# Kernel tuning notes

Measured on AMD Instinct MI355X. Metric: run time of the kernel, lower is better.

The kernel has to match this reference:

```python
import jax, jax.numpy as jnp
import numpy as np

N_NODES = 100000
DEGREE = 16
FEAT = 128
HID = 64
OUT = 16
BATCH = 4096
K = 12  # n_neibs


def setup_inputs() -> dict:
    key = jax.random.key(0)
    ks = jax.random.split(key, 12)
    idx0 = jax.random.randint(ks[0], (BATCH,), 0, N_NODES, dtype=jnp.int64 if jax.config.jax_enable_x64 else jnp.int32)
    buf1 = jax.random.randint(ks[1], (BATCH, K), 0, 1000000)
    buf2 = jax.random.randint(ks[2], (BATCH * K, K), 0, 1000000)
    indptr = jnp.arange(N_NODES) * DEGREE            # CSR row pointers (fixed degree)
    indices = jax.random.randint(ks[3], (N_NODES * DEGREE,), 0, N_NODES)
    degrees = jnp.full((N_NODES,), DEGREE, dtype=jnp.int32)
    emb_weight = jax.random.normal(ks[4], (N_NODES, FEAT), dtype=jnp.float32)
    enc_w = jax.random.normal(ks[5], (HID, FEAT), dtype=jnp.float32) * (1.0 / np.sqrt(FEAT))
    h1_w = jax.random.normal(ks[6], (HID, 2 * HID), dtype=jnp.float32) * (1.0 / np.sqrt(2 * HID))
    h1_b = jnp.zeros((HID,), jnp.float32)
    h2_w = jax.random.normal(ks[7], (HID, HID), dtype=jnp.float32) * (1.0 / np.sqrt(HID))
    h2_b = jnp.zeros((HID,), jnp.float32)
    out_w = jax.random.normal(ks[8], (OUT, HID), dtype=jnp.float32) * (1.0 / np.sqrt(HID))
    out_b = jnp.zeros((OUT,), jnp.float32)
    return dict(idx0=idx0, buf1=buf1, buf2=buf2, indptr=indptr, indices=indices,
                degrees=degrees, emb_weight=emb_weight, enc_w=enc_w,
                h1_w=h1_w, h1_b=h1_b, h2_w=h2_w, h2_b=h2_b, out_w=out_w, out_b=out_b)


def _sample_neighbors(nodes, buf, indptr, indices, degrees):
    # nodes: [M], buf: [M, K] random ints -> neighbor node ids [M, K]
    neibs = buf % degrees[nodes][:, None]
    offsets = indptr[nodes][:, None] + neibs
    return indices[offsets]


def reference(idx0, buf1, buf2, indptr, indices, degrees, emb_weight,
              enc_w, h1_w, h1_b, h2_w, h2_b, out_w, out_b):
    B = idx0.shape[0]
    idx1 = _sample_neighbors(idx0, buf1, indptr, indices, degrees)              # [B, K]
    idx2 = _sample_neighbors(idx1.reshape(B * K), buf2, indptr, indices, degrees)
    idx2 = idx2.reshape(B, K, K)                                                # [B, K, K]

    enc_1hop = jax.nn.relu(jnp.einsum('bkf,hf->bkh', emb_weight[idx1], enc_w))  # [B, K, H]
    enc_2hop = jax.nn.relu(jnp.einsum('bkjf,hf->bkjh', emb_weight[idx2], enc_w))
    avg_2hop = enc_2hop.mean(axis=-2)                                           # [B, K, H]

    h1 = jnp.concatenate([enc_1hop, avg_2hop], axis=-1)                         # [B, K, 2H]
    h1 = jax.nn.relu(jnp.einsum('bkc,hc->bkh', h1, h1_w) + h1_b)
    avg_1hop = h1.mean(axis=-2)                                                 # [B, H]
    h0 = jax.nn.relu(avg_1hop @ h2_w.T + h2_b)
    return h0 @ out_w.T + out_b                                                 # [B, OUT]
```

## Files before the change

kernel.cpp:

```cpp
#include <hip/hip_runtime.h>

#define NNODES 100000

typedef __attribute__((ext_vector_type(8))) short bf16x8;
typedef __attribute__((ext_vector_type(4))) float floatx4;

union PackU { uint4 u; bf16x8 v; };

__device__ __forceinline__ uint pack_hi2(float x0, float x1) {
    return (__float_as_uint(x1) & 0xFFFF0000u) | (__float_as_uint(x0) >> 16);
}
__device__ __forceinline__ uint pack_lo2(float x0, float x1) {
    float l0 = x0 - __uint_as_float(__float_as_uint(x0) & 0xFFFF0000u);
    float l1 = x1 - __uint_as_float(__float_as_uint(x1) & 0xFFFF0000u);
    return (__float_as_uint(l1) & 0xFFFF0000u) | (__float_as_uint(l0) >> 16);
}
__device__ __forceinline__ ushort bf_rne(float x) {
    unsigned u = __float_as_uint(x);
    return (ushort)((u + 0x7FFFu + ((u >> 16) & 1u)) >> 16);
}
__device__ __forceinline__ float lo16f(uint u) { return __uint_as_float(u << 16); }
__device__ __forceinline__ float hi16f(uint u) { return __uint_as_float(u & 0xFFFF0000u); }

__global__ __launch_bounds__(256) void k_prep(const float* __restrict__ enc_w,
                                              const float* __restrict__ h1_w,
                                              uint4* __restrict__ frgB,
                                              uint4* __restrict__ frgW) {
    const int t = threadIdx.x;
#pragma unroll
    for (int r = 0; r < 8; ++r) {
        int id = t + 256 * r;
        int lane = id & 63, m = lane & 15, q = lane >> 4;
        if (id < 1024) {
            int ks = (id >> 6) & 3, ht = id >> 8;
            const float* p = enc_w + (ht * 16 + m) * 128 + ks * 32 + q * 8;
            float4 f0 = *(const float4*)p, f1 = *(const float4*)(p + 4);
            frgB[((ht * 4 + ks) * 2 + 0) * 64 + lane] =
                (uint4){pack_hi2(f0.x, f0.y), pack_hi2(f0.z, f0.w),
                        pack_hi2(f1.x, f1.y), pack_hi2(f1.z, f1.w)};
            frgB[((ht * 4 + ks) * 2 + 1) * 64 + lane] =
                (uint4){pack_lo2(f0.x, f0.y), pack_lo2(f0.z, f0.w),
                        pack_lo2(f1.x, f1.y), pack_lo2(f1.z, f1.w)};
        } else {
            int id2 = id - 1024;
            int ks = (id2 >> 6) & 1, ot = id2 >> 7;
            int o2 = ot * 16 + m;
            const float* p = h1_w + (o2 & 63) * 128 + (o2 & 64) + ks * 32 + q * 8;
            float4 f0 = *(const float4*)p, f1 = *(const float4*)(p + 4);
            frgW[((ot * 2 + ks) * 2 + 0) * 64 + lane] =
                (uint4){pack_hi2(f0.x, f0.y), pack_hi2(f0.z, f0.w),
                        pack_hi2(f1.x, f1.y), pack_hi2(f1.z, f1.w)};
            frgW[((ot * 2 + ks) * 2 + 1) * 64 + lane] =
                (uint4){pack_lo2(f0.x, f0.y), pack_lo2(f0.z, f0.w),
                        pack_lo2(f1.x, f1.y), pack_lo2(f1.z, f1.w)};
        }
    }
}

__global__ __launch_bounds__(256, 4) void k_gemm(const float* __restrict__ emb,
                                                 const uint4* __restrict__ frgB,
                                                 const uint4* __restrict__ frgW,
                                                 ushort* __restrict__ encAB) {
    __shared__ ushort sE[2 * 64 * 72];
    const int t = threadIdx.x;
    const int n0 = blockIdx.x * 64;
    const int w = t >> 6, lane = t & 63;
    const int m = lane & 15, q = lane >> 4;

    int nn = n0 + w * 16 + m; if (nn > NNODES - 1) nn = NNODES - 1;
    const float* rowp = emb + (size_t)nn * 128 + q * 8;
    bf16x8 a_h[4], a_l[4];
#pragma unroll
    for (int ks = 0; ks < 4; ++ks) {
        float4 f0 = *(const float4*)(rowp + ks * 32);
        float4 f1 = *(const float4*)(rowp + ks * 32 + 4);
        PackU ph, pl;
        ph.u = (uint4){pack_hi2(f0.x, f0.y), pack_hi2(f0.z, f0.w),
                       pack_hi2(f1.x, f1.y), pack_hi2(f1.z, f1.w)};
        pl.u = (uint4){pack_lo2(f0.x, f0.y), pack_lo2(f0.z, f0.w),
                       pack_lo2(f1.x, f1.y), pack_lo2(f1.z, f1.w)};
        a_h[ks] = ph.v; a_l[ks] = pl.v;
    }

    const uint4* pB = frgB + lane;
    floatx4 acc[4] = {};
#pragma unroll
    for (int ht = 0; ht < 4; ++ht) {
#pragma unroll
        for (int ks = 0; ks < 4; ++ks) {
            PackU bh, bl;
            bh.u = pB[((ht * 4 + ks) * 2 + 0) * 64];
            bl.u = pB[((ht * 4 + ks) * 2 + 1) * 64];
            acc[ht] = __builtin_amdgcn_mfma_f32_16x16x32_bf16(a_h[ks], bh.v, acc[ht], 0, 0, 0);
            acc[ht] = __builtin_amdgcn_mfma_f32_16x16x32_bf16(a_l[ks], bh.v, acc[ht], 0, 0, 0);
            acc[ht] = __builtin_amdgcn_mfma_f32_16x16x32_bf16(a_h[ks], bl.v, acc[ht], 0, 0, 0);
        }
    }

#pragma unroll
    for (int ht = 0; ht < 4; ++ht)
#pragma unroll
        for (int i = 0; i < 4; ++i) {
            float v = fmaxf(acc[ht][i], 0.f);
            int row = w * 16 + q * 4 + i, col = ht * 16 + m;
            uint uv = __float_as_uint(v);
            sE[row * 72 + col] = (ushort)(uv >> 16);
            float lo = v - __uint_as_float(uv & 0xFFFF0000u);
            sE[64 * 72 + row * 72 + col] = (ushort)(__float_as_uint(lo) >> 16);
        }
    __syncthreads();

    bf16x8 e_h[2], e_l[2];
    {
        const ushort* pE = sE + (w * 16 + m) * 72 + q * 8;
#pragma unroll
        for (int ks = 0; ks < 2; ++ks) {
            e_h[ks] = *(const bf16x8*)(pE + ks * 32);
            e_l[ks] = *(const bf16x8*)(pE + 64 * 72 + ks * 32);
        }
    }
    const uint4* pW = frgW + lane;
    floatx4 acc2[8] = {};
#pragma unroll
    for (int ot = 0; ot < 8; ++ot) {
#pragma unroll
        for (int ks = 0; ks < 2; ++ks) {
            PackU wh, wl;
            wh.u = pW[((ot * 2 + ks) * 2 + 0) * 64];
            wl.u = pW[((ot * 2 + ks) * 2 + 1) * 64];
            acc2[ot] = __builtin_amdgcn_mfma_f32_16x16x32_bf16(e_h[ks], wh.v, acc2[ot], 0, 0, 0);
            acc2[ot] = __builtin_amdgcn_mfma_f32_16x16x32_bf16(e_l[ks], wh.v, acc2[ot], 0, 0, 0);
            acc2[ot] = __builtin_amdgcn_mfma_f32_16x16x32_bf16(e_h[ks], wl.v, acc2[ot], 0, 0, 0);
        }
    }
#pragma unroll
    for (int ot = 0; ot < 8; ++ot)
#pragma unroll
        for (int i = 0; i < 4; ++i) {
            int n = n0 + w * 16 + q * 4 + i;
            if (n < NNODES) encAB[n * 128 + ot * 16 + m] = bf_rne(acc2[ot][i]);
        }
}

__global__ __launch_bounds__(256) void k_gather_head(const int* __restrict__ idx0,
                                                     const int* __restrict__ buf1,
                                                     const int* __restrict__ buf2,
                                                     const int* __restrict__ indices,
                                                     const ushort* __restrict__ encAB,
                                                     const float* __restrict__ h1_b,
                                                     const float* __restrict__ h2_w,
                                                     const float* __restrict__ h2_b,
                                                     const float* __restrict__ out_w,
                                                     const float* __restrict__ out_b,
                                                     float* __restrict__ out) {
    __shared__ int s_idx1[48];
    __shared__ int s_idx2[576];
    __shared__ float sW2[64 * 65];
    __shared__ float sWo[64 * 17];
    __shared__ float sAvg[4][64];
    __shared__ float sH0[4][64];

    const int t = threadIdx.x;
    const int b0 = blockIdx.x * 4;

    if (t < 48) {
        int bl = t / 12;
        s_idx1[t] = indices[idx0[b0 + bl] * 16 + (buf1[b0 * 12 + t] & 15)];
    }
#pragma unroll
    for (int r = 0; r < 16; ++r) {
        int e = t + 256 * r;
        sW2[(e & 63) * 65 + (e >> 6)] = h2_w[e];
    }
#pragma unroll
    for (int r = 0; r < 4; ++r) {
        int e = t + 256 * r;
        sWo[(e & 63) * 17 + (e >> 6)] = out_w[e];
    }
    __syncthreads();

#pragma unroll
    for (int r = 0; r < 3; ++r) {
        int s = t + 256 * r;
        if (s < 576) {
            int bk = s / 12;
            s_idx2[s] = indices[s_idx1[bk] * 16 + (buf2[b0 * 144 + s] & 15)];
        }
    }
    __syncthreads();

    const int w = t >> 6, lane = t & 63;
    const int pp = lane >> 5, c = lane & 31;
    const uint* __restrict__ encAB32 = (const uint*)encAB;
    const int* myi1 = &s_idx1[w * 12];
    const int* myi2 = &s_idx2[w * 144];
    float2 bb = *(const float2*)&h1_b[2 * c];
    float hs0 = 0.f, hs1 = 0.f;
#pragma unroll 3
    for (int k = 0; k < 12; ++k) {
        uint av = encAB32[myi1[k] * 64 + c];
        float s0 = 0.f, s1 = 0.f;
#pragma unroll
        for (int jj = 0; jj < 6; ++jj) {
            uint v = encAB32[myi2[k * 12 + 2 * jj + pp] * 64 + 32 + c];
            s0 += lo16f(v); s1 += hi16f(v);
        }
        s0 += __shfl_xor(s0, 32);
        s1 += __shfl_xor(s1, 32);
        hs0 += fmaxf(lo16f(av) + s0 * (1.f / 12.f) + bb.x, 0.f);
        hs1 += fmaxf(hi16f(av) + s1 * (1.f / 12.f) + bb.y, 0.f);
    }
    if (pp == 0) {
        sAvg[w][2 * c]     = hs0 * (1.f / 12.f);
        sAvg[w][2 * c + 1] = hs1 * (1.f / 12.f);
    }
    __syncthreads();

    {
        float acc = h2_b[lane];
#pragma unroll 8
        for (int i = 0; i < 64; ++i)
            acc += sAvg[w][i] * sW2[i * 65 + lane];
        sH0[w][lane] = fmaxf(acc, 0.f);
    }
    __syncthreads();
    if (t < 64) {
        int g2 = t >> 4, o = t & 15;
        float acc2 = out_b[o];
#pragma unroll 8
        for (int i = 0; i < 64; ++i)
            acc2 += sH0[g2][i] * sWo[i * 17 + o];
        out[(b0 + g2) * 16 + o] = acc2;
    }
}

extern "C" void kernel_launch(void* const* d_in, const int* in_sizes, int n_in,
                              void* d_out, int out_size, void* d_ws, size_t ws_size,
                              hipStream_t stream) {
    const int*   idx0    = (const int*)d_in[0];
    const int*   buf1    = (const int*)d_in[1];
    const int*   buf2    = (const int*)d_in[2];
    const int*   indices = (const int*)d_in[4];
    const float* emb     = (const float*)d_in[6];
    const float* enc_w   = (const float*)d_in[7];
    const float* h1_w    = (const float*)d_in[8];
    const float* h1_b    = (const float*)d_in[9];
    const float* h2_w    = (const float*)d_in[10];
    const float* h2_b    = (const float*)d_in[11];
    const float* out_w   = (const float*)d_in[12];
    const float* out_b   = (const float*)d_in[13];
    (void)d_in[3]; (void)d_in[5];
    float* out = (float*)d_out;

    ushort* encAB = (ushort*)d_ws;
    uint4* frgB = (uint4*)((char*)d_ws + 25600000);
    uint4* frgW = frgB + 2048;

    k_prep<<<1, 256, 0, stream>>>(enc_w, h1_w, frgB, frgW);
    k_gemm<<<1563, 256, 0, stream>>>(emb, frgB, frgW, encAB);
    k_gather_head<<<1024, 256, 0, stream>>>(idx0, buf1, buf2, indices, encAB,
                                            h1_b, h2_w, h2_b, out_w, out_b, out);
}
```

Baseline: 151.4 us.

## Fuse prep, GEMM and gather kernels into one cooperative persistent kernel

```diff
diff --git a/kernel.cpp b/kernel.cpp
--- a/kernel.cpp
+++ b/kernel.cpp
@@ -1,4 +1,7 @@
 #include <hip/hip_runtime.h>
+#include <hip/hip_cooperative_groups.h>
+
+namespace cg = cooperative_groups;
 
 #define NNODES 100000
 
@@ -22,10 +25,23 @@
 __device__ __forceinline__ float lo16f(uint u) { return __uint_as_float(u << 16); }
 __device__ __forceinline__ float hi16f(uint u) { return __uint_as_float(u & 0xFFFF0000u); }
 
-__global__ __launch_bounds__(256) void k_prep(const float* __restrict__ enc_w,
-                                              const float* __restrict__ h1_w,
-                                              uint4* __restrict__ frgB,
-                                              uint4* __restrict__ frgW) {
+struct GatherSM {
+    int idx1[48];
+    int idx2[576];
+    float W2[64 * 65];
+    float Wo[64 * 17];
+    float Avg[4][64];
+    float H0[4][64];
+};
+union FusedSM {
+    ushort sE[2 * 64 * 72];
+    GatherSM g;
+};
+
+__device__ __forceinline__ void prep_frags(const float* __restrict__ enc_w,
+                                           const float* __restrict__ h1_w,
+                                           uint4* __restrict__ frgB,
+                                           uint4* __restrict__ frgW) {
     const int t = threadIdx.x;
 #pragma unroll
     for (int r = 0; r < 8; ++r) {
@@ -57,13 +73,12 @@
     }
 }
 
-__global__ __launch_bounds__(256, 4) void k_gemm(const float* __restrict__ emb,
-                                                 const uint4* __restrict__ frgB,
-                                                 const uint4* __restrict__ frgW,
-                                                 ushort* __restrict__ encAB) {
-    __shared__ ushort sE[2 * 64 * 72];
+__device__ __forceinline__ void gemm_tile(int n0, const float* __restrict__ emb,
+                                          const uint4* __restrict__ frgB,
+                                          const uint4* __restrict__ frgW,
+                                          ushort* __restrict__ encAB,
+                                          ushort* sE) {
     const int t = threadIdx.x;
-    const int n0 = blockIdx.x * 64;
     const int w = t >> 6, lane = t & 63;
     const int m = lane & 15, q = lane >> 4;
 
@@ -140,8 +155,141 @@
             int n = n0 + w * 16 + q * 4 + i;
             if (n < NNODES) encAB[n * 128 + ot * 16 + m] = bf_rne(acc2[ot][i]);
         }
-}
-
+    __syncthreads();
+}
+
+__device__ __forceinline__ void gather_quad(int b0, GatherSM& g,
+                                            const int* __restrict__ idx0,
+                                            const int* __restrict__ buf1,
+                                            const int* __restrict__ buf2,
+                                            const int* __restrict__ indices,
+                                            const ushort* __restrict__ encAB,
+                                            const float* __restrict__ h1_b,
+                                            const float* __restrict__ h2_w,
+                                            const float* __restrict__ h2_b,
+                                            const float* __restrict__ out_w,
+                                            const float* __restrict__ out_b,
+                                            float* __restrict__ out) {
+    const int t = threadIdx.x;
+
+    if (t < 48) {
+        int bl = t / 12;
+        g.idx1[t] = indices[idx0[b0 + bl] * 16 + (buf1[b0 * 12 + t] & 15)];
+    }
+#pragma unroll
+    for (int r = 0; r < 16; ++r) {
+        int e = t + 256 * r;
+        g.W2[(e & 63) * 65 + (e >> 6)] = h2_w[e];
+    }
+#pragma unroll
+    for (int r = 0; r < 4; ++r) {
+        int e = t + 256 * r;
+        g.Wo[(e & 63) * 17 + (e >> 6)] = out_w[e];
+    }
+    __syncthreads();
+
+#pragma unroll
+    for (int r = 0; r < 3; ++r) {
+        int s = t + 256 * r;
+        if (s < 576) {
+            int bk = s / 12;
+            g.idx2[s] = indices[g.idx1[bk] * 16 + (buf2[b0 * 144 + s] & 15)];
+        }
+    }
+    __syncthreads();
+
+    const int w = t >> 6, lane = t & 63;
+    const int pp = lane >> 5, c = lane & 31;
+    const uint* __restrict__ encAB32 = (const uint*)encAB;
+    const int* myi1 = &g.idx1[w * 12];
+    const int* myi2 = &g.idx2[w * 144];
+    float2 bb = *(const float2*)&h1_b[2 * c];
+    float hs0 = 0.f, hs1 = 0.f;
+#pragma unroll 3
+    for (int k = 0; k < 12; ++k) {
+        uint av = encAB32[myi1[k] * 64 + c];
+        float s0 = 0.f, s1 = 0.f;
+#pragma unroll
+        for (int jj = 0; jj < 6; ++jj) {
+            uint v = encAB32[myi2[k * 12 + 2 * jj + pp] * 64 + 32 + c];
+            s0 += lo16f(v); s1 += hi16f(v);
+        }
+        s0 += __shfl_xor(s0, 32);
+        s1 += __shfl_xor(s1, 32);
+        hs0 += fmaxf(lo16f(av) + s0 * (1.f / 12.f) + bb.x, 0.f);
+        hs1 += fmaxf(hi16f(av) + s1 * (1.f / 12.f) + bb.y, 0.f);
+    }
+    if (pp == 0) {
+        g.Avg[w][2 * c]     = hs0 * (1.f / 12.f);
+        g.Avg[w][2 * c + 1] = hs1 * (1.f / 12.f);
+    }
+    __syncthreads();
+
+    {
+        float acc = h2_b[lane];
+#pragma unroll 8
+        for (int i = 0; i < 64; ++i)
+            acc += g.Avg[w][i] * g.W2[i * 65 + lane];
+        g.H0[w][lane] = fmaxf(acc, 0.f);
+    }
+    __syncthreads();
+    if (t < 64) {
+        int g2 = t >> 4, o = t & 15;
+        float acc2 = out_b[o];
+#pragma unroll 8
+        for (int i = 0; i < 64; ++i)
+            acc2 += g.H0[g2][i] * g.Wo[i * 17 + o];
+        out[(b0 + g2) * 16 + o] = acc2;
+    }
+    __syncthreads();
+}
+
+__global__ __launch_bounds__(256, 4) void k_fused(const float* __restrict__ emb,
+                                                  const float* __restrict__ enc_w,
+                                                  const float* __restrict__ h1_w,
+                                                  const uint4* __restrict__ frgB,
+                                                  const uint4* __restrict__ frgW,
+                                                  ushort* __restrict__ encAB,
+                                                  const int* __restrict__ idx0,
+                                                  const int* __restrict__ buf1,
+                                                  const int* __restrict__ buf2,
+                                                  const int* __restrict__ indices,
+                                                  const float* __restrict__ h1_b,
+                                                  const float* __restrict__ h2_w,
+                                                  const float* __restrict__ h2_b,
+                                                  const float* __restrict__ out_w,
+                                                  const float* __restrict__ out_b,
+                                                  float* __restrict__ out) {
+    __shared__ FusedSM sm;
+
+    if (blockIdx.x == 0)
+        prep_frags(enc_w, h1_w, const_cast<uint4*>(frgB), const_cast<uint4*>(frgW));
+    __threadfence();
+    cg::this_grid().sync();
+
+    for (int tile = blockIdx.x; tile < 1563; tile += gridDim.x)
+        gemm_tile(tile * 64, emb, frgB, frgW, encAB, sm.sE);
+    __threadfence();
+    cg::this_grid().sync();
+
+    for (int qb = blockIdx.x; qb < 1024; qb += gridDim.x)
+        gather_quad(qb * 4, sm.g, idx0, buf1, buf2, indices, encAB,
+                    h1_b, h2_w, h2_b, out_w, out_b, out);
+}
+
+__global__ __launch_bounds__(256) void k_prep(const float* __restrict__ enc_w,
+                                              const float* __restrict__ h1_w,
+                                              uint4* __restrict__ frgB,
+                                              uint4* __restrict__ frgW) {
+    prep_frags(enc_w, h1_w, frgB, frgW);
+}
+__global__ __launch_bounds__(256, 4) void k_gemm(const float* __restrict__ emb,
+                                                 const uint4* __restrict__ frgB,
+                                                 const uint4* __restrict__ frgW,
+                                                 ushort* __restrict__ encAB) {
+    __shared__ ushort sE[2 * 64 * 72];
+    gemm_tile(blockIdx.x * 64, emb, frgB, frgW, encAB, sE);
+}
 __global__ __launch_bounds__(256) void k_gather_head(const int* __restrict__ idx0,
                                                      const int* __restrict__ buf1,
                                                      const int* __restrict__ buf2,
@@ -153,85 +301,9 @@
                                                      const float* __restrict__ out_w,
                                                      const float* __restrict__ out_b,
                                                      float* __restrict__ out) {
-    __shared__ int s_idx1[48];
-    __shared__ int s_idx2[576];
-    __shared__ float sW2[64 * 65];
-    __shared__ float sWo[64 * 17];
-    __shared__ float sAvg[4][64];
-    __shared__ float sH0[4][64];
-
-    const int t = threadIdx.x;
-    const int b0 = blockIdx.x * 4;
-
-    if (t < 48) {
-        int bl = t / 12;
-        s_idx1[t] = indices[idx0[b0 + bl] * 16 + (buf1[b0 * 12 + t] & 15)];
-    }
-#pragma unroll
-    for (int r = 0; r < 16; ++r) {
-        int e = t + 256 * r;
-        sW2[(e & 63) * 65 + (e >> 6)] = h2_w[e];
-    }
-#pragma unroll
-    for (int r = 0; r < 4; ++r) {
-        int e = t + 256 * r;
-        sWo[(e & 63) * 17 + (e >> 6)] = out_w[e];
-    }
-    __syncthreads();
-
-#pragma unroll
-    for (int r = 0; r < 3; ++r) {
-        int s = t + 256 * r;
-        if (s < 576) {
-            int bk = s / 12;
-            s_idx2[s] = indices[s_idx1[bk] * 16 + (buf2[b0 * 144 + s] & 15)];
-        }
-    }
-    __syncthreads();
-
-    const int w = t >> 6, lane = t & 63;
-    const int pp = lane >> 5, c = lane & 31;
-    const uint* __restrict__ encAB32 = (const uint*)encAB;
-    const int* myi1 = &s_idx1[w * 12];
-    const int* myi2 = &s_idx2[w * 144];
-    float2 bb = *(const float2*)&h1_b[2 * c];
-    float hs0 = 0.f, hs1 = 0.f;
-#pragma unroll 3
-    for (int k = 0; k < 12; ++k) {
-        uint av = encAB32[myi1[k] * 64 + c];
-        float s0 = 0.f, s1 = 0.f;
-#pragma unroll
-        for (int jj = 0; jj < 6; ++jj) {
-            uint v = encAB32[myi2[k * 12 + 2 * jj + pp] * 64 + 32 + c];
-            s0 += lo16f(v); s1 += hi16f(v);
-        }
-        s0 += __shfl_xor(s0, 32);
-        s1 += __shfl_xor(s1, 32);
-        hs0 += fmaxf(lo16f(av) + s0 * (1.f / 12.f) + bb.x, 0.f);
-        hs1 += fmaxf(hi16f(av) + s1 * (1.f / 12.f) + bb.y, 0.f);
-    }
-    if (pp == 0) {
-        sAvg[w][2 * c]     = hs0 * (1.f / 12.f);
-        sAvg[w][2 * c + 1] = hs1 * (1.f / 12.f);
-    }
-    __syncthreads();
-
-    {
-        float acc = h2_b[lane];
-#pragma unroll 8
-        for (int i = 0; i < 64; ++i)
-            acc += sAvg[w][i] * sW2[i * 65 + lane];
-        sH0[w][lane] = fmaxf(acc, 0.f);
-    }
-    __syncthreads();
-    if (t < 64) {
-        int g2 = t >> 4, o = t & 15;
-        float acc2 = out_b[o];
-#pragma unroll 8
-        for (int i = 0; i < 64; ++i)
-            acc2 += sH0[g2][i] * sWo[i * 17 + o];
-        out[(b0 + g2) * 16 + o] = acc2;
-    }
+    __shared__ GatherSM g;
+    gather_quad(blockIdx.x * 4, g, idx0, buf1, buf2, indices, encAB,
+                h1_b, h2_w, h2_b, out_w, out_b, out);
 }
 
 extern "C" void kernel_launch(void* const* d_in, const int* in_sizes, int n_in,
@@ -256,8 +328,26 @@
     uint4* frgB = (uint4*)((char*)d_ws + 25600000);
     uint4* frgW = frgB + 2048;
 
-    k_prep<<<1, 256, 0, stream>>>(enc_w, h1_w, frgB, frgW);
-    k_gemm<<<1563, 256, 0, stream>>>(emb, frgB, frgW, encAB);
-    k_gather_head<<<1024, 256, 0, stream>>>(idx0, buf1, buf2, indices, encAB,
-                                            h1_b, h2_w, h2_b, out_w, out_b, out);
-}
+    static int nblk = 0;
+    if (nblk == 0) {
+        int perCU = 0;
+        if (hipOccupancyMaxActiveBlocksPerMultiprocessor(&perCU, (const void*)k_fused, 256, 0)
+                != hipSuccess || perCU <= 0)
+            perCU = 4;
+        nblk = perCU * 256;
+        if (nblk > 1024) nblk = 1024;
+    }
+
+    void* kargs[] = {(void*)&emb, (void*)&enc_w, (void*)&h1_w, (void*)&frgB, (void*)&frgW,
+                     (void*)&encAB, (void*)&idx0, (void*)&buf1, (void*)&buf2, (void*)&indices,
+                     (void*)&h1_b, (void*)&h2_w, (void*)&h2_b, (void*)&out_w, (void*)&out_b,
+                     (void*)&out};
+    hipError_t e = hipLaunchCooperativeKernel((const void*)k_fused, dim3(nblk), dim3(256),
+                                              kargs, 0, stream);
+    if (e != hipSuccess) {
+        k_prep<<<1, 256, 0, stream>>>(enc_w, h1_w, frgB, frgW);
+        k_gemm<<<1563, 256, 0, stream>>>(emb, frgB, frgW, encAB);
+        k_gather_head<<<1024, 256, 0, stream>>>(idx0, buf1, buf2, indices, encAB,
+                                                h1_b, h2_w, h2_b, out_w, out_b, out);
+    }
+}
```

Result: slower. 405.5 us (+167.8%).
